# Kernel optimization log

Measured on AMD Instinct MI355X. Metric: run time of the kernel, lower is better.

The kernel has to match this reference:

```python
import jax, jax.numpy as jnp
import numpy as np

# dims: layers, batch, seq_len, num_nodes, n_experts, top_k, expert hidden, pred_len
LAYERS, B, L, N, E, K, DFF, P = 3, 32, 336, 321, 4, 2, 512, 96
LOSS_COEF = 0.01
INV_SQRT2 = 0.7071067811865476


def setup_inputs() -> dict:
    key = jax.random.key(0)
    ks = jax.random.split(key, 10)
    w = lambda k, shape: (jax.random.normal(k, shape, jnp.float32) * 0.02)
    return {
        "x": jax.random.normal(ks[0], (B, L, N, 1), jnp.float32),
        "noise": jax.random.normal(ks[1], (LAYERS, B, E), jnp.float32),
        "w_gate": w(ks[2], (LAYERS, L, E)),
        "w_noise": w(ks[3], (LAYERS, L, E)),
        "W1": w(ks[4], (LAYERS, E, L, DFF)),
        "b1": jnp.zeros((LAYERS, E, DFF), jnp.float32),
        "W2": w(ks[5], (LAYERS, E, DFF, L)),
        "b2": jnp.zeros((LAYERS, E, L), jnp.float32),
        "p1w": w(ks[6], (P, L)),
        "p1b": jnp.zeros((P,), jnp.float32),
        "p2w": w(ks[7], (2 * P, P)),
        "p2b": jnp.zeros((2 * P,), jnp.float32),
    }


def _cv_sq(v):
    # squared coefficient of variation (unbiased var, matches torch .var())
    return jnp.var(v, ddof=1) / (jnp.mean(v) ** 2 + 1e-10)


def _norm_cdf(z):
    return 0.5 * (1.0 + jax.lax.erf(z * jnp.asarray(INV_SQRT2, z.dtype)))


def _ams_layer(x, noise, wg, wn, W1, b1, W2, b2):
    # x: [B, L, N] -> [B, L, N]; noisy top-k gated MoE over the time axis
    g = x.mean(axis=2)                                   # [B, L] gate features
    clean = g @ wg                                       # [B, E]
    nstd = jax.nn.softplus(g @ wn) + 1e-2                # [B, E]
    noisy = clean + noise * nstd                         # [B, E]

    top_logits, top_idx = jax.lax.top_k(noisy, K + 1)    # [B, K+1]
    gates_k = jax.nn.softmax(top_logits[:, :K], axis=-1)
    gates = jnp.zeros_like(noisy).at[
        jnp.arange(noisy.shape[0])[:, None], top_idx[:, :K]
    ].set(gates_k)                                       # dense [B, E], zeros off top-k

    importance = gates.sum(axis=0)
    thr_in = top_logits[:, K][:, None]                   # (k+1)-th value
    thr_out = top_logits[:, K - 1][:, None]              # k-th value
    is_in = noisy > thr_in
    load = jnp.where(
        is_in,
        _norm_cdf((clean - thr_in) / nstd),
        _norm_cdf((clean - thr_out) / nstd),
    ).sum(axis=0)
    aux = LOSS_COEF * (_cv_sq(importance) + _cv_sq(load))

    # experts: per-node MLP along time dim, evaluated densely and combined by gates
    xT = x.transpose(0, 2, 1)                            # [B, N, L]
    h = jax.nn.gelu(jnp.einsum('bnl,eld->ebnd', xT, W1) + b1[:, None, None, :])
    y = jnp.einsum('ebnd,edl->ebnl', h, W2) + b2[:, None, None, :]
    out = jnp.einsum('be,ebnl->bln', gates, y) + x       # residual connection
    return out, aux


def reference(x, noise, w_gate, w_noise, W1, b1, W2, b2, p1w, p1b, p2w, p2b):
    x0 = x[..., 0]                                       # [B, L, N]
    # RevIN norm (affine=False): per-sample, per-node stats over time
    mu = x0.mean(axis=1, keepdims=True)
    sd = jnp.sqrt(x0.var(axis=1, keepdims=True) + 1e-5)
    out = (x0 - mu) / sd

    balance_loss = jnp.asarray(0.0, jnp.float32)
    for l in range(LAYERS):
        out, aux = _ams_layer(out, noise[l], w_gate[l], w_noise[l],
                              W1[l], b1[l], W2[l], b2[l])
        balance_loss = balance_loss + aux

    # projection head: [B, N, L] -> [B, N, 2P] -> [B, P, N, 2]
    h = jnp.tanh(out.transpose(0, 2, 1) @ p1w.T + p1b)
    proj = (h @ p2w.T + p2b).reshape(out.shape[0], N, P, 2).transpose(0, 2, 1, 3)
    mean_out = proj[..., 0]
    std_out = jax.nn.softplus(proj[..., 1]) + 1e-6
    return mean_out, balance_loss, std_out
```

## Files before the change

kernel.cpp:

```cpp
#include <hip/hip_runtime.h>
#include <hip/hip_bf16.h>

#define NLAYERS 3
#define BB 32
#define LL 336
#define LP 352
#define NN 321
#define EE 4
#define DHID 512
#define PP 96
#define STOT (BB*NN*LL)
#define MROWS (BB*NN)
#define BPN ((size_t)BB*PP*NN)

#define F1S 5632
#define E1S 180224
#define F2S 8192
#define E2S 172032

typedef __attribute__((ext_vector_type(8))) short short8;
typedef __attribute__((ext_vector_type(4))) float float4v;

union BF { __hip_bfloat16 h; short s; };

__device__ __forceinline__ short f2b(float f) { BF u; u.h = __float2bfloat16(f); return u.s; }

__device__ __forceinline__ float fast_tanh(float y) {
    float e = __expf(2.0f * y);
    return 1.0f - 2.0f / (e + 1.0f);
}
__device__ __forceinline__ float gelu_f(float x) {
    return 0.5f * x * (1.0f + fast_tanh(0.7978845608028654f * (x + 0.044715f * x * x * x)));
}
__device__ __forceinline__ float softplus_f(float x) {
    return fmaxf(x, 0.0f) + log1pf(expf(-fabsf(x)));
}

__global__ __launch_bounds__(256) void prep_kernel(
    const float* __restrict__ x, const float* __restrict__ W1, const float* __restrict__ W2,
    const float* __restrict__ p1w, const float* __restrict__ p2w,
    float* __restrict__ MU, float* __restrict__ IV, float* __restrict__ LOSS,
    float* __restrict__ G0, short* __restrict__ W1f, short* __restrict__ W2f,
    short* __restrict__ p1wb, short* __restrict__ p2wb)
{
    __shared__ short Ws[64][72];
    __shared__ float Ss[4][64], Sq[4][64];
    int idx = blockIdx.x, tid = threadIdx.x;
    if (idx < 1152) {
        const float* src; int K, D, KS, bx, by, le;
        if (idx < 576) {
            le = idx / 48; int r = idx % 48;
            src = W1 + (size_t)le * LL * DHID;
            K = LL; D = DHID; KS = LP; bx = r % 8; by = r / 8;
        } else {
            int s2 = idx - 576; le = s2 / 48; int r = s2 % 48;
            src = W2 + (size_t)le * DHID * LL;
            K = DHID; D = LL; KS = DHID; bx = r % 6; by = r / 6;
        }
        int d0 = bx * 64, k0 = by * 64;
        #pragma unroll
        for (int i = 0; i < 16; ++i) {
            int lin = tid + i * 256;
            int ki = lin >> 6, dj = lin & 63;
            int k = k0 + ki, d = d0 + dj;
            Ws[ki][dj] = (k < K && d < D) ? f2b(src[(size_t)k * D + d]) : (short)0;
        }
        __syncthreads();
        int di = tid >> 2, d = d0 + di;
        if (d >= D) return;
        #pragma unroll
        for (int kp = 0; kp < 2; ++kp) {
            int kj = ((tid & 3) + 4 * kp) * 8;
            int k = k0 + kj;
            if (k >= KS) continue;
            union { short s[8]; uint4 u; } pk;
            #pragma unroll
            for (int j = 0; j < 8; ++j) pk.s[j] = Ws[kj + j][di];
            int nf = d >> 4;
            int ks = k >> 5;
            int l  = (((k >> 3) & 3) << 4) | (d & 15);
            if (idx < 576) {
                size_t o = (size_t)le * E1S + ((size_t)(nf * 11 + ks) * 64 + l) * 8;
                *(uint4*)&W1f[o] = pk.u;
            } else {
                size_t o = (size_t)le * E2S + ((size_t)(nf * 16 + ks) * 64 + l) * 8;
                *(uint4*)&W2f[o] = pk.u;
            }
        }
    } else if (idx < 1344) {
        int q = idx - 1152;
        int b = q / 6, nt = q % 6;
        if (tid < 56) G0[q * 56 + tid] = 0.0f;
        if (q == 0 && tid < 8) LOSS[tid] = 0.0f;
        int ni = tid & 63, lc = tid >> 6;
        int n = nt * 64 + ni;
        float s = 0.f, ss = 0.f;
        if (n < NN) {
            const float* xp = x + ((size_t)b * LL + lc * 84) * NN + n;
            for (int l = 0; l < 84; ++l, xp += NN) {
                float v = *xp; s += v; ss = fmaf(v, v, ss);
            }
        }
        Ss[lc][ni] = s; Sq[lc][ni] = ss;
        __syncthreads();
        if (lc == 0 && n < NN) {
            float st = ((Ss[0][ni] + Ss[1][ni]) + Ss[2][ni]) + Ss[3][ni];
            float sq = ((Sq[0][ni] + Sq[1][ni]) + Sq[2][ni]) + Sq[3][ni];
            float mu  = st * (1.0f / LL);
            float var = sq * (1.0f / LL) - mu * mu;
            MU[b * NN + n] = mu;
            IV[b * NN + n] = 1.0f / sqrtf(var + 1e-5f);
        }
    } else {
        int i = (idx - 1344) * 256 + tid;
        if (i < PP * LP) {
            int n = i / LP, k = i - n * LP;
            p1wb[i] = (k < LL) ? f2b(p1w[n * LL + k]) : (short)0;
        } else if (i < PP * LP + 2 * PP * PP) {
            int j = i - PP * LP;
            p2wb[j] = f2b(p2w[j]);
        }
    }
}

__global__ __launch_bounds__(256) void revin_tn(
    const float* __restrict__ x, const float* __restrict__ MU, const float* __restrict__ IV,
    float* __restrict__ T, short* __restrict__ Tb16, float* __restrict__ G0)
{
    int b = blockIdx.x, nt = blockIdx.y, lt = blockIdx.z;
    int n0 = nt * 64, l0 = lt * 48;
    __shared__ float Ls[48][65];
    __shared__ float Vs[48][65];
    int tid = threadIdx.x;
    #pragma unroll
    for (int i = 0; i < 12; ++i) {
        int lin = tid + i * 256;
        int li = lin >> 6, ni = lin & 63;
        int n = n0 + ni;
        Ls[li][ni] = (n < NN) ? x[((size_t)b * LL + l0 + li) * NN + n] : 0.f;
    }
    __syncthreads();
    int r = tid >> 2, q = tid & 3;
    int n = n0 + r;
    bool valid = (n < NN);
    float mu = 0.f, iv = 0.f;
    if (valid) { mu = MU[b * NN + n]; iv = IV[b * NN + n]; }
    size_t rowf = (size_t)(b * NN + (valid ? n : 0)) * LL + l0;
    size_t rowb = (size_t)(b * NN + (valid ? n : 0)) * LP + l0;
    #pragma unroll
    for (int k = 0; k < 3; ++k) {
        int c = (q + 4 * k) * 4;
        float4 v;
        v.x = (Ls[c    ][r] - mu) * iv;
        v.y = (Ls[c + 1][r] - mu) * iv;
        v.z = (Ls[c + 2][r] - mu) * iv;
        v.w = (Ls[c + 3][r] - mu) * iv;
        Vs[c][r] = v.x; Vs[c + 1][r] = v.y; Vs[c + 2][r] = v.z; Vs[c + 3][r] = v.w;
        if (valid) {
            *(float4*)&T[rowf + c] = v;
            union { short s[4]; uint2 u; } pk;
            pk.s[0] = f2b(v.x); pk.s[1] = f2b(v.y); pk.s[2] = f2b(v.z); pk.s[3] = f2b(v.w);
            *(uint2*)&Tb16[rowb + c] = pk.u;
        }
    }
    if (valid && lt == 6 && q == 3) {
        size_t base = (size_t)(b * NN + n) * LP;
        *(uint4*)&Tb16[base + 336] = make_uint4(0, 0, 0, 0);
        *(uint4*)&Tb16[base + 344] = make_uint4(0, 0, 0, 0);
    }
    __syncthreads();
    if (tid < 48) {
        float s = 0.f;
        #pragma unroll 8
        for (int rr = 0; rr < 64; ++rr) s += Vs[tid][rr];
        unsafeAtomicAdd(&G0[b * LL + l0 + tid], s);
    }
}

struct LossSM {
    float pc2[BB][EE][2], pn2[BB][EE][2];
    float sc[BB][EE], sn[BB][EE], sy[BB][EE], sg[BB][EE];
    float sti[BB], sto[BB];
    float simp[EE], sload[EE];
};

__device__ void loss_tail(LossSM* S, const float* __restrict__ Gcur, float* __restrict__ Gnext,
                          const float* __restrict__ wgL, const float* __restrict__ wnL,
                          const float* __restrict__ noiseL, float* __restrict__ LOSS, int tid)
{
    __syncthreads();
    for (int t = tid; t < BB * LL; t += 256) Gnext[t] = 0.0f;
    {
        int bb = tid >> 3, ee = (tid >> 1) & 3, sub = tid & 1;
        float c = 0.f, nr = 0.f;
        const float* gp = Gcur + bb * LL;
        for (int l = sub * 168; l < sub * 168 + 168; ++l) {
            float gv = gp[l] * (1.0f / NN);
            c  = fmaf(gv, wgL[l * EE + ee], c);
            nr = fmaf(gv, wnL[l * EE + ee], nr);
        }
        S->pc2[bb][ee][sub] = c; S->pn2[bb][ee][sub] = nr;
    }
    __syncthreads();
    if (tid < 128) {
        int bb = tid >> 2, ee = tid & 3;
        float c  = S->pc2[bb][ee][0] + S->pc2[bb][ee][1];
        float nr = S->pn2[bb][ee][0] + S->pn2[bb][ee][1];
        float ns = softplus_f(nr) + 1e-2f;
        S->sc[bb][ee] = c; S->sn[bb][ee] = ns;
        S->sy[bb][ee] = fmaf(noiseL[bb * EE + ee], ns, c);
    }
    __syncthreads();
    if (tid < 128 && (tid & 3) == 0) {
        int bb = tid >> 2;
        float v[4];
        #pragma unroll
        for (int i = 0; i < 4; ++i) v[i] = S->sy[bb][i];
        int i0 = 0;
        for (int i = 1; i < 4; ++i) if (v[i] > v[i0]) i0 = i;
        int i1 = -1;
        for (int i = 0; i < 4; ++i) { if (i == i0) continue; if (i1 < 0 || v[i] > v[i1]) i1 = i; }
        float m3 = -1e30f;
        for (int i = 0; i < 4; ++i) { if (i == i0 || i == i1) continue; if (v[i] > m3) m3 = v[i]; }
        float e1 = expf(v[i1] - v[i0]);
        float invd = 1.0f / (1.0f + e1);
        #pragma unroll
        for (int i = 0; i < 4; ++i) S->sg[bb][i] = 0.f;
        S->sg[bb][i0] = invd;
        S->sg[bb][i1] = e1 * invd;
        S->sti[bb] = m3;
        S->sto[bb] = v[i1];
    }
    __syncthreads();
    if (tid < EE) {
        int ee = tid;
        float imp = 0.f, ld = 0.f;
        for (int bb2 = 0; bb2 < BB; ++bb2) {
            imp += S->sg[bb2][ee];
            float thr = (S->sy[bb2][ee] > S->sti[bb2]) ? S->sti[bb2] : S->sto[bb2];
            float z = (S->sc[bb2][ee] - thr) / S->sn[bb2][ee];
            ld += 0.5f * (1.0f + erff(z * 0.7071067811865476f));
        }
        S->simp[ee] = imp; S->sload[ee] = ld;
    }
    __syncthreads();
    if (tid == 0) {
        float aux = 0.f;
        {
            float m = (S->simp[0] + S->simp[1] + S->simp[2] + S->simp[3]) * 0.25f;
            float var = 0.f;
            for (int i = 0; i < 4; ++i) { float d = S->simp[i] - m; var += d * d; }
            var *= (1.0f / 3.0f);
            aux += var / (m * m + 1e-10f);
        }
        {
            float m = (S->sload[0] + S->sload[1] + S->sload[2] + S->sload[3]) * 0.25f;
            float var = 0.f;
            for (int i = 0; i < 4; ++i) { float d = S->sload[i] - m; var += d * d; }
            var *= (1.0f / 3.0f);
            aux += var / (m * m + 1e-10f);
        }
        LOSS[0] += 0.01f * aux;
    }
}

__global__ __launch_bounds__(256, 3) void fc1_mfma(
    const short* __restrict__ Tb16, const short* __restrict__ W1f_l,
    const float* __restrict__ b1_l,
    const float* __restrict__ Gcur, float* __restrict__ Gnext,
    const float* __restrict__ wgL, const float* __restrict__ wnL,
    const float* __restrict__ noiseL,
    int* __restrict__ IDX, float* __restrict__ GV,
    short* __restrict__ Hs, float* __restrict__ LOSS)
{
    int i = blockIdx.x;
    int low = i & 7, rest = i >> 3;
    int v = rest & 3, ghi = rest >> 2;
    int g = ghi * 8 + low;
    int y = g % 6, b = g / 6;
    int xt = v & 1, slot = v >> 1;
    int m0 = y * 64, n0 = xt * 256;
    int tid = threadIdx.x;
    int wave = tid >> 6, lane = tid & 63, quad = lane >> 4, l16 = lane & 15;
    __shared__ __align__(16) short Al[64][360];
    __shared__ int sE[2];
    __shared__ float sGt[2];
    {
        int r = tid >> 2, c0 = (tid & 3) * 8;
        const short* src = Tb16 + ((size_t)b * NN + m0 + r) * LP + c0;
        #pragma unroll
        for (int ks = 0; ks < 11; ++ks)
            *(uint4*)&Al[r][c0 + ks * 32] = *(const uint4*)(src + ks * 32);
    }
    if (tid < 64) {
        float pc[4] = {0.f,0.f,0.f,0.f}, pn[4] = {0.f,0.f,0.f,0.f};
        const float* gp = Gcur + b * LL;
        for (int l = tid; l < LL; l += 64) {
            float gv = gp[l] * (1.0f / NN);
            #pragma unroll
            for (int e2 = 0; e2 < 4; ++e2) {
                pc[e2] = fmaf(gv, wgL[l * EE + e2], pc[e2]);
                pn[e2] = fmaf(gv, wnL[l * EE + e2], pn[e2]);
            }
        }
        #pragma unroll
        for (int off = 32; off >= 1; off >>= 1) {
            #pragma unroll
            for (int e2 = 0; e2 < 4; ++e2) {
                pc[e2] += __shfl_xor(pc[e2], off);
                pn[e2] += __shfl_xor(pn[e2], off);
            }
        }
        if (tid == 0) {
            float vv[4];
            #pragma unroll
            for (int e2 = 0; e2 < 4; ++e2) {
                float ns = softplus_f(pn[e2]) + 1e-2f;
                vv[e2] = fmaf(noiseL[b * EE + e2], ns, pc[e2]);
            }
            int i0 = 0;
            for (int e2 = 1; e2 < 4; ++e2) if (vv[e2] > vv[i0]) i0 = e2;
            int i1 = -1;
            for (int e2 = 0; e2 < 4; ++e2) { if (e2 == i0) continue; if (i1 < 0 || vv[e2] > vv[i1]) i1 = e2; }
            float e1v = expf(vv[i1] - vv[i0]);
            float invd = 1.0f / (1.0f + e1v);
            sE[0] = i0; sE[1] = i1; sGt[0] = invd; sGt[1] = e1v * invd;
        }
    }
    __syncthreads();
    int e = sE[slot];
    float gt = sGt[slot];
    if (y == 0 && v == 0 && tid < 2) {
        IDX[2 * b + tid] = sE[tid];
        GV[2 * b + tid] = sGt[tid];
    }

    const short* Bf = W1f_l + (size_t)(e * 32 + xt * 16 + wave * 4) * F1S + lane * 8;
    float4v zero4 = {0.f, 0.f, 0.f, 0.f};
    float4v acc[4][4];
    #pragma unroll
    for (int a = 0; a < 4; ++a)
        #pragma unroll
        for (int j = 0; j < 4; ++j) acc[a][j] = zero4;

    short8 bc0 = *(const short8*)(Bf);
    short8 bc1 = *(const short8*)(Bf + F1S);
    short8 bc2 = *(const short8*)(Bf + 2 * F1S);
    short8 bc3 = *(const short8*)(Bf + 3 * F1S);
    #pragma unroll
    for (int ks = 0; ks < 11; ++ks) {
        short8 bn0, bn1, bn2, bn3;
        if (ks < 10) {
            int o = (ks + 1) * 512;
            bn0 = *(const short8*)(Bf + o);
            bn1 = *(const short8*)(Bf + F1S + o);
            bn2 = *(const short8*)(Bf + 2 * F1S + o);
            bn3 = *(const short8*)(Bf + 3 * F1S + o);
        }
        int off = ks * 32;
        short8 af[4];
        #pragma unroll
        for (int mi = 0; mi < 4; ++mi) af[mi] = *(const short8*)&Al[mi * 16 + l16][off + quad * 8];
        #pragma unroll
        for (int mi = 0; mi < 4; ++mi) {
            acc[mi][0] = __builtin_amdgcn_mfma_f32_16x16x32_bf16(af[mi], bc0, acc[mi][0], 0, 0, 0);
            acc[mi][1] = __builtin_amdgcn_mfma_f32_16x16x32_bf16(af[mi], bc1, acc[mi][1], 0, 0, 0);
            acc[mi][2] = __builtin_amdgcn_mfma_f32_16x16x32_bf16(af[mi], bc2, acc[mi][2], 0, 0, 0);
            acc[mi][3] = __builtin_amdgcn_mfma_f32_16x16x32_bf16(af[mi], bc3, acc[mi][3], 0, 0, 0);
        }
        if (ks < 10) { bc0 = bn0; bc1 = bn1; bc2 = bn2; bc3 = bn3; }
    }
    const float* bb = b1_l + (size_t)e * DHID;
    int wn4 = wave * 64;
    float bias[4];
    #pragma unroll
    for (int ni = 0; ni < 4; ++ni) bias[ni] = bb[n0 + wn4 + ni * 16 + l16];
    short* Ho = Hs + (size_t)(b * 2 + slot) * NN * DHID;
    #pragma unroll
    for (int mi = 0; mi < 4; ++mi) {
        #pragma unroll
        for (int r = 0; r < 4; ++r) {
            int gm = m0 + mi * 16 + quad * 4 + r;
            if (gm >= NN) continue;
            #pragma unroll
            for (int ni = 0; ni < 4; ++ni) {
                int gd = n0 + wn4 + ni * 16 + l16;
                float vv = acc[mi][ni][r] + bias[ni];
                Ho[(size_t)gm * DHID + gd] = f2b(gt * gelu_f(vv));
            }
        }
    }
    if (i == 0) loss_tail((LossSM*)&Al[0][0], Gcur, Gnext, wgL, wnL, noiseL, LOSS, tid);
}

__global__ __launch_bounds__(256, 4) void fc2_fused(
    const short* __restrict__ Hs, const short* __restrict__ W2f_l,
    const float* __restrict__ b2_l, float* __restrict__ T,
    short* __restrict__ Tb16, float* __restrict__ Gnext,
    const int* __restrict__ IDX, const float* __restrict__ GV, int lastL)
{
    int i = blockIdx.x;
    int low = i & 7, rest = i >> 3;
    int v = rest % 3, ghi = rest / 3;
    int g = ghi * 8 + low;
    int y = g % 6, b = g / 6;
    int m0 = y * 64, n0 = v * 128;
    int tid = threadIdx.x;
    int wave = tid >> 6, lane = tid & 63, quad = lane >> 4, l16 = lane & 15;
    int wn = wave * 32;
    __shared__ short Al[64][264];
    int e0 = IDX[2 * b], e1 = IDX[2 * b + 1];
    float gt0 = GV[2 * b], gt1 = GV[2 * b + 1];
    float4v zero4 = {0.f, 0.f, 0.f, 0.f};
    float4v acc[4][2];
    #pragma unroll
    for (int a = 0; a < 4; ++a)
        #pragma unroll
        for (int j = 0; j < 2; ++j) acc[a][j] = zero4;

    int nfr = v * 8 + wave * 2;
    int nf0 = (nfr > 20) ? 20 : nfr;
    int nf1 = (nfr + 1 > 20) ? 20 : nfr + 1;

    int r8 = tid >> 5, c0s = (tid & 31) * 8;
    #pragma unroll
    for (int sc2 = 0; sc2 < 4; ++sc2) {
        int slot = sc2 >> 1, chunk = sc2 & 1;
        int koff = chunk * 256;
        int ez = slot ? e1 : e0;
        const short* As = Hs + ((size_t)(b * 2 + slot) * NN + m0) * DHID + koff;
        #pragma unroll
        for (int a = 0; a < 8; ++a)
            *(uint4*)&Al[a * 8 + r8][c0s] = *(const uint4*)(As + (size_t)(a * 8 + r8) * DHID + c0s);
        __syncthreads();
        const short* B0 = W2f_l + (size_t)ez * E2S + (size_t)nf0 * F2S + (size_t)chunk * 8 * 512 + lane * 8;
        const short* B1 = W2f_l + (size_t)ez * E2S + (size_t)nf1 * F2S + (size_t)chunk * 8 * 512 + lane * 8;
        short8 c0 = *(const short8*)(B0);
        short8 c1 = *(const short8*)(B1);
        #pragma unroll
        for (int ks = 0; ks < 8; ++ks) {
            short8 n0v, n1v;
            if (ks < 7) {
                n0v = *(const short8*)(B0 + (ks + 1) * 512);
                n1v = *(const short8*)(B1 + (ks + 1) * 512);
            }
            int off = ks * 32;
            short8 af[4];
            #pragma unroll
            for (int mi = 0; mi < 4; ++mi) af[mi] = *(const short8*)&Al[mi * 16 + l16][off + quad * 8];
            #pragma unroll
            for (int mi = 0; mi < 4; ++mi) {
                acc[mi][0] = __builtin_amdgcn_mfma_f32_16x16x32_bf16(af[mi], c0, acc[mi][0], 0, 0, 0);
                acc[mi][1] = __builtin_amdgcn_mfma_f32_16x16x32_bf16(af[mi], c1, acc[mi][1], 0, 0, 0);
            }
            if (ks < 7) { c0 = n0v; c1 = n1v; }
        }
        __syncthreads();
    }
    const float* b2e0 = b2_l + (size_t)e0 * LL;
    const float* b2e1 = b2_l + (size_t)e1 * LL;
    float* Tb = T + (size_t)b * NN * LL;
    short* Bt = Tb16 + (size_t)b * NN * LP;
    #pragma unroll
    for (int ni = 0; ni < 2; ++ni) {
        int gl = n0 + wn + ni * 16 + l16;
        float s = 0.f;
        if (gl < LL) {
            float bias = gt0 * b2e0[gl] + gt1 * b2e1[gl];
            #pragma unroll
            for (int mi = 0; mi < 4; ++mi) {
                #pragma unroll
                for (int r = 0; r < 4; ++r) {
                    int gm = m0 + mi * 16 + quad * 4 + r;
                    if (gm < NN) {
                        float vv = acc[mi][ni][r] + bias + Tb[(size_t)gm * LL + gl];
                        if (!lastL) Tb[(size_t)gm * LL + gl] = vv;
                        Bt[(size_t)gm * LP + gl] = f2b(vv);
                        s += vv;
                    }
                }
            }
        }
        s += __shfl_xor(s, 16);
        s += __shfl_xor(s, 32);
        if (!lastL && quad == 0 && gl < LL)
            unsafeAtomicAdd(&Gnext[b * LL + gl], s);
    }
}

__global__ __launch_bounds__(256) void proj_fused(
    const short* __restrict__ Tb16,
    const short* __restrict__ p1wb, const float* __restrict__ p1b,
    const short* __restrict__ p2wb, const float* __restrict__ p2b,
    float* __restrict__ out, const float* __restrict__ LOSS)
{
    __shared__ short Al[32][360];
    __shared__ short Hp[32][104];
    int m0 = blockIdx.x * 32;
    int tid = threadIdx.x;
    if (blockIdx.x == 0 && tid == 0) out[BPN] = LOSS[0];
    int wave = tid >> 6, lane = tid & 63, quad = lane >> 4, l16 = lane & 15;
    float4v zero4 = {0.f, 0.f, 0.f, 0.f};

    #pragma unroll
    for (int i = 0; i < 6; ++i) {
        int idx = tid + i * 256;
        if (idx < 1408) {
            int r = idx / 44, c = (idx - r * 44) * 8;
            *(uint4*)&Al[r][c] = *(const uint4*)(Tb16 + (size_t)(m0 + r) * LP + c);
        }
    }
    __syncthreads();

    {
        int rf = wave & 1, cfb = wave >> 1;
        float4v acc1[3];
        #pragma unroll
        for (int j = 0; j < 3; ++j) acc1[j] = zero4;
        const short* B1p0 = p1wb + (size_t)(cfb * 16 + l16) * LP + quad * 8;
        #pragma unroll
        for (int ks = 0; ks < 11; ++ks) {
            int off = ks * 32;
            short8 af = *(const short8*)&Al[rf * 16 + l16][off + quad * 8];
            #pragma unroll
            for (int j = 0; j < 3; ++j) {
                short8 bf = *(const short8*)(B1p0 + (size_t)j * 32 * LP + off);
                acc1[j] = __builtin_amdgcn_mfma_f32_16x16x32_bf16(af, bf, acc1[j], 0, 0, 0);
            }
        }
        #pragma unroll
        for (int j = 0; j < 3; ++j) {
            int p = (cfb + 2 * j) * 16 + l16;
            float pb = p1b[p];
            #pragma unroll
            for (int r = 0; r < 4; ++r)
                Hp[rf * 16 + quad * 4 + r][p] = f2b(fast_tanh(acc1[j][r] + pb));
        }
    }
    __syncthreads();

    float4v acc2[3][2];
    #pragma unroll
    for (int a = 0; a < 3; ++a)
        #pragma unroll
        for (int j = 0; j < 2; ++j) acc2[a][j] = zero4;
    #pragma unroll
    for (int kc = 0; kc < 3; ++kc) {
        int off = kc * 32 + quad * 8;
        short8 bfv0 = *(const short8*)&Hp[l16][off];
        short8 bfv1 = *(const short8*)&Hp[16 + l16][off];
        #pragma unroll
        for (int mi = 0; mi < 3; ++mi) {
            int cf = wave * 3 + mi;
            short8 af = *(const short8*)(p2wb + (size_t)(cf * 16 + l16) * PP + off);
            acc2[mi][0] = __builtin_amdgcn_mfma_f32_16x16x32_bf16(af, bfv0, acc2[mi][0], 0, 0, 0);
            acc2[mi][1] = __builtin_amdgcn_mfma_f32_16x16x32_bf16(af, bfv1, acc2[mi][1], 0, 0, 0);
        }
    }
    int bqv[2], ndv[2];
    #pragma unroll
    for (int ni = 0; ni < 2; ++ni) {
        int gm = m0 + ni * 16 + l16;
        int bq = gm / NN;
        bqv[ni] = bq; ndv[ni] = gm - bq * NN;
    }
    #pragma unroll
    for (int mi = 0; mi < 3; ++mi) {
        #pragma unroll
        for (int r = 0; r < 4; ++r) {
            int c = (wave * 3 + mi) * 16 + quad * 4 + r;
            float pb = p2b[c];
            int p = c >> 1;
            if ((r & 1) == 0) {
                #pragma unroll
                for (int ni = 0; ni < 2; ++ni) {
                    float v = acc2[mi][ni][r] + pb;
                    out[((size_t)bqv[ni] * PP + p) * NN + ndv[ni]] = v;
                }
            } else {
                #pragma unroll
                for (int ni = 0; ni < 2; ++ni) {
                    float v = acc2[mi][ni][r] + pb;
                    out[BPN + 1 + ((size_t)bqv[ni] * PP + p) * NN + ndv[ni]] = softplus_f(v) + 1e-6f;
                }
            }
        }
    }
}

extern "C" void kernel_launch(void* const* d_in, const int* in_sizes, int n_in,
                              void* d_out, int out_size, void* d_ws, size_t ws_size,
                              hipStream_t stream)
{
    const float* x     = (const float*)d_in[0];
    const float* noise = (const float*)d_in[1];
    const float* wg    = (const float*)d_in[2];
    const float* wn    = (const float*)d_in[3];
    const float* W1    = (const float*)d_in[4];
    const float* b1    = (const float*)d_in[5];
    const float* W2    = (const float*)d_in[6];
    const float* b2    = (const float*)d_in[7];
    const float* p1w   = (const float*)d_in[8];
    const float* p1b   = (const float*)d_in[9];
    const float* p2w   = (const float*)d_in[10];
    const float* p2b   = (const float*)d_in[11];
    float* out = (float*)d_out;

    float* ws   = (float*)d_ws;
    float* T    = ws;
    float* G0   = T + STOT;
    float* G1   = G0 + BB * LL;
    float* LOSS = G1 + BB * LL;
    float* GV   = LOSS + 8;
    int*   IDX  = (int*)(GV + 64);
    float* MU   = (float*)(IDX + 64);
    float* IV   = MU + MROWS;
    short* W1f  = (short*)(IV + MROWS);
    short* W2f  = W1f + (size_t)NLAYERS * EE * DHID * LP;
    short* p1wb = W2f + (size_t)NLAYERS * EE * LL * DHID;
    short* p2wb = p1wb + PP * LP;
    short* Tb16 = p2wb + 2 * PP * PP;
    short* Hs   = Tb16 + (size_t)(MROWS + 64) * LP;

    prep_kernel<<<1549, 256, 0, stream>>>(x, W1, W2, p1w, p2w, MU, IV, LOSS, G0,
                                          W1f, W2f, p1wb, p2wb);
    revin_tn<<<dim3(BB, 6, 7), 256, 0, stream>>>(x, MU, IV, T, Tb16, G0);

    for (int l = 0; l < NLAYERS; ++l) {
        const float* Gcur = (l == 1) ? G1 : G0;
        float* Gnext      = (l == 1) ? G0 : G1;
        fc1_mfma<<<768, 256, 0, stream>>>(
            Tb16, W1f + (size_t)l * EE * E1S, b1 + (size_t)l * EE * DHID,
            Gcur, Gnext, wg + (size_t)l * LL * EE, wn + (size_t)l * LL * EE,
            noise + (size_t)l * BB * EE, IDX, GV, Hs, LOSS);
        fc2_fused<<<576, 256, 0, stream>>>(
            Hs, W2f + (size_t)l * EE * E2S, b2 + (size_t)l * EE * LL,
            T, Tb16, Gnext, IDX, GV, (l == NLAYERS - 1) ? 1 : 0);
    }
    proj_fused<<<321, 256, 0, stream>>>(Tb16, p1wb, p1b, p2wb, p2b, out, LOSS);
}
```

Measured before the change: 347.1 us.

## Parallelize gate reduction and deepen prefetch pipelines in both MoE GEMM kernels

The gate-logit reduction in the first expert GEMM now uses all four waves with a shared-memory cross-wave sum instead of a single wave, and every thread computes top-k redundantly rather than waiting on one thread. The W1 and W2 B-fragment loads are prefetched two k-steps ahead instead of one. In the second GEMM the next A-tile chunk is loaded into registers while the current chunk's MFMAs run, then written to LDS. This is meant to hide global-load latency and shorten the serial gate prologue, at the cost of more registers, which may reduce occupancy.

```diff
diff --git a/kernel.cpp b/kernel.cpp
--- a/kernel.cpp
+++ b/kernel.cpp
@@ -283,8 +283,7 @@
     int tid = threadIdx.x;
     int wave = tid >> 6, lane = tid & 63, quad = lane >> 4, l16 = lane & 15;
     __shared__ __align__(16) short Al[64][360];
-    __shared__ int sE[2];
-    __shared__ float sGt[2];
+    __shared__ float redc[4][4], redn[4][4];
     {
         int r = tid >> 2, c0 = (tid & 3) * 8;
         const short* src = Tb16 + ((size_t)b * NN + m0 + r) * LP + c0;
@@ -292,47 +291,59 @@
         for (int ks = 0; ks < 11; ++ks)
             *(uint4*)&Al[r][c0 + ks * 32] = *(const uint4*)(src + ks * 32);
     }
-    if (tid < 64) {
-        float pc[4] = {0.f,0.f,0.f,0.f}, pn[4] = {0.f,0.f,0.f,0.f};
+    {
+        float pce[4] = {0.f,0.f,0.f,0.f}, pne[4] = {0.f,0.f,0.f,0.f};
         const float* gp = Gcur + b * LL;
-        for (int l = tid; l < LL; l += 64) {
-            float gv = gp[l] * (1.0f / NN);
+        #pragma unroll
+        for (int pass = 0; pass < 2; ++pass) {
+            int l = tid + pass * 256;
+            if (l < LL) {
+                float gv = gp[l] * (1.0f / NN);
+                #pragma unroll
+                for (int e2 = 0; e2 < 4; ++e2) {
+                    pce[e2] = fmaf(gv, wgL[l * EE + e2], pce[e2]);
+                    pne[e2] = fmaf(gv, wnL[l * EE + e2], pne[e2]);
+                }
+            }
+        }
+        #pragma unroll
+        for (int off = 32; off >= 1; off >>= 1) {
             #pragma unroll
             for (int e2 = 0; e2 < 4; ++e2) {
-                pc[e2] = fmaf(gv, wgL[l * EE + e2], pc[e2]);
-                pn[e2] = fmaf(gv, wnL[l * EE + e2], pn[e2]);
-            }
-        }
-        #pragma unroll
-        for (int off = 32; off >= 1; off >>= 1) {
-            #pragma unroll
-            for (int e2 = 0; e2 < 4; ++e2) {
-                pc[e2] += __shfl_xor(pc[e2], off);
-                pn[e2] += __shfl_xor(pn[e2], off);
-            }
-        }
-        if (tid == 0) {
-            float vv[4];
-            #pragma unroll
-            for (int e2 = 0; e2 < 4; ++e2) {
-                float ns = softplus_f(pn[e2]) + 1e-2f;
-                vv[e2] = fmaf(noiseL[b * EE + e2], ns, pc[e2]);
-            }
-            int i0 = 0;
-            for (int e2 = 1; e2 < 4; ++e2) if (vv[e2] > vv[i0]) i0 = e2;
-            int i1 = -1;
-            for (int e2 = 0; e2 < 4; ++e2) { if (e2 == i0) continue; if (i1 < 0 || vv[e2] > vv[i1]) i1 = e2; }
-            float e1v = expf(vv[i1] - vv[i0]);
-            float invd = 1.0f / (1.0f + e1v);
-            sE[0] = i0; sE[1] = i1; sGt[0] = invd; sGt[1] = e1v * invd;
-        }
-    }
-    __syncthreads();
-    int e = sE[slot];
-    float gt = sGt[slot];
-    if (y == 0 && v == 0 && tid < 2) {
-        IDX[2 * b + tid] = sE[tid];
-        GV[2 * b + tid] = sGt[tid];
+                pce[e2] += __shfl_xor(pce[e2], off);
+                pne[e2] += __shfl_xor(pne[e2], off);
+            }
+        }
+        if (lane == 0) {
+            #pragma unroll
+            for (int e2 = 0; e2 < 4; ++e2) { redc[wave][e2] = pce[e2]; redn[wave][e2] = pne[e2]; }
+        }
+    }
+    __syncthreads();
+    int e; float gt;
+    {
+        float vv[4];
+        #pragma unroll
+        for (int e2 = 0; e2 < 4; ++e2) {
+            float c  = ((redc[0][e2] + redc[1][e2]) + redc[2][e2]) + redc[3][e2];
+            float nr = ((redn[0][e2] + redn[1][e2]) + redn[2][e2]) + redn[3][e2];
+            float ns = softplus_f(nr) + 1e-2f;
+            vv[e2] = fmaf(noiseL[b * EE + e2], ns, c);
+        }
+        int i0 = 0;
+        #pragma unroll
+        for (int e2 = 1; e2 < 4; ++e2) if (vv[e2] > vv[i0]) i0 = e2;
+        int i1 = -1;
+        #pragma unroll
+        for (int e2 = 0; e2 < 4; ++e2) { if (e2 == i0) continue; if (i1 < 0 || vv[e2] > vv[i1]) i1 = e2; }
+        float e1v = expf(vv[i1] - vv[i0]);
+        float invd = 1.0f / (1.0f + e1v);
+        e  = slot ? i1 : i0;
+        gt = slot ? (e1v * invd) : invd;
+        if (y == 0 && v == 0 && tid == 0) {
+            IDX[2 * b] = i0; IDX[2 * b + 1] = i1;
+            GV[2 * b] = invd; GV[2 * b + 1] = e1v * invd;
+        }
     }
 
     const short* Bf = W1f_l + (size_t)(e * 32 + xt * 16 + wave * 4) * F1S + lane * 8;
@@ -343,19 +354,18 @@
         #pragma unroll
         for (int j = 0; j < 4; ++j) acc[a][j] = zero4;
 
-    short8 bc0 = *(const short8*)(Bf);
-    short8 bc1 = *(const short8*)(Bf + F1S);
-    short8 bc2 = *(const short8*)(Bf + 2 * F1S);
-    short8 bc3 = *(const short8*)(Bf + 3 * F1S);
+    short8 bc[4], bd[4];
+    #pragma unroll
+    for (int j = 0; j < 4; ++j) bc[j] = *(const short8*)(Bf + j * F1S);
+    #pragma unroll
+    for (int j = 0; j < 4; ++j) bd[j] = *(const short8*)(Bf + j * F1S + 512);
     #pragma unroll
     for (int ks = 0; ks < 11; ++ks) {
-        short8 bn0, bn1, bn2, bn3;
-        if (ks < 10) {
-            int o = (ks + 1) * 512;
-            bn0 = *(const short8*)(Bf + o);
-            bn1 = *(const short8*)(Bf + F1S + o);
-            bn2 = *(const short8*)(Bf + 2 * F1S + o);
-            bn3 = *(const short8*)(Bf + 3 * F1S + o);
+        short8 bn[4];
+        if (ks < 9) {
+            int o = (ks + 2) * 512;
+            #pragma unroll
+            for (int j = 0; j < 4; ++j) bn[j] = *(const short8*)(Bf + j * F1S + o);
         }
         int off = ks * 32;
         short8 af[4];
@@ -363,12 +373,13 @@
         for (int mi = 0; mi < 4; ++mi) af[mi] = *(const short8*)&Al[mi * 16 + l16][off + quad * 8];
         #pragma unroll
         for (int mi = 0; mi < 4; ++mi) {
-            acc[mi][0] = __builtin_amdgcn_mfma_f32_16x16x32_bf16(af[mi], bc0, acc[mi][0], 0, 0, 0);
-            acc[mi][1] = __builtin_amdgcn_mfma_f32_16x16x32_bf16(af[mi], bc1, acc[mi][1], 0, 0, 0);
-            acc[mi][2] = __builtin_amdgcn_mfma_f32_16x16x32_bf16(af[mi], bc2, acc[mi][2], 0, 0, 0);
-            acc[mi][3] = __builtin_amdgcn_mfma_f32_16x16x32_bf16(af[mi], bc3, acc[mi][3], 0, 0, 0);
-        }
-        if (ks < 10) { bc0 = bn0; bc1 = bn1; bc2 = bn2; bc3 = bn3; }
+            acc[mi][0] = __builtin_amdgcn_mfma_f32_16x16x32_bf16(af[mi], bc[0], acc[mi][0], 0, 0, 0);
+            acc[mi][1] = __builtin_amdgcn_mfma_f32_16x16x32_bf16(af[mi], bc[1], acc[mi][1], 0, 0, 0);
+            acc[mi][2] = __builtin_amdgcn_mfma_f32_16x16x32_bf16(af[mi], bc[2], acc[mi][2], 0, 0, 0);
+            acc[mi][3] = __builtin_amdgcn_mfma_f32_16x16x32_bf16(af[mi], bc[3], acc[mi][3], 0, 0, 0);
+        }
+        #pragma unroll
+        for (int j = 0; j < 4; ++j) { bc[j] = bd[j]; if (ks < 9) bd[j] = bn[j]; }
     }
     const float* bb = b1_l + (size_t)e * DHID;
     int wn4 = wave * 64;
@@ -423,26 +434,40 @@
     int nf1 = (nfr + 1 > 20) ? 20 : nfr + 1;
 
     int r8 = tid >> 5, c0s = (tid & 31) * 8;
+    uint4 areg[8];
+    {
+        const short* As = Hs + ((size_t)(b * 2 + 0) * NN + m0) * DHID + 0;
+        #pragma unroll
+        for (int a = 0; a < 8; ++a)
+            areg[a] = *(const uint4*)(As + (size_t)(a * 8 + r8) * DHID + c0s);
+        #pragma unroll
+        for (int a = 0; a < 8; ++a)
+            *(uint4*)&Al[a * 8 + r8][c0s] = areg[a];
+    }
+    __syncthreads();
     #pragma unroll
     for (int sc2 = 0; sc2 < 4; ++sc2) {
         int slot = sc2 >> 1, chunk = sc2 & 1;
-        int koff = chunk * 256;
         int ez = slot ? e1 : e0;
-        const short* As = Hs + ((size_t)(b * 2 + slot) * NN + m0) * DHID + koff;
-        #pragma unroll
-        for (int a = 0; a < 8; ++a)
-            *(uint4*)&Al[a * 8 + r8][c0s] = *(const uint4*)(As + (size_t)(a * 8 + r8) * DHID + c0s);
-        __syncthreads();
-        const short* B0 = W2f_l + (size_t)ez * E2S + (size_t)nf0 * F2S + (size_t)chunk * 8 * 512 + lane * 8;
-        const short* B1 = W2f_l + (size_t)ez * E2S + (size_t)nf1 * F2S + (size_t)chunk * 8 * 512 + lane * 8;
-        short8 c0 = *(const short8*)(B0);
-        short8 c1 = *(const short8*)(B1);
+        if (sc2 < 3) {
+            int nslot = (sc2 + 1) >> 1, nchunk = (sc2 + 1) & 1;
+            const short* Asn = Hs + ((size_t)(b * 2 + nslot) * NN + m0) * DHID + nchunk * 256;
+            #pragma unroll
+            for (int a = 0; a < 8; ++a)
+                areg[a] = *(const uint4*)(Asn + (size_t)(a * 8 + r8) * DHID + c0s);
+        }
+        const short* B0 = W2f_l + (size_t)ez * E2S + (size_t)nf0 * F2S + (size_t)chunk * 4096 + lane * 8;
+        const short* B1 = W2f_l + (size_t)ez * E2S + (size_t)nf1 * F2S + (size_t)chunk * 4096 + lane * 8;
+        short8 c0v = *(const short8*)(B0);
+        short8 c1v = *(const short8*)(B1);
+        short8 d0v = *(const short8*)(B0 + 512);
+        short8 d1v = *(const short8*)(B1 + 512);
         #pragma unroll
         for (int ks = 0; ks < 8; ++ks) {
             short8 n0v, n1v;
-            if (ks < 7) {
-                n0v = *(const short8*)(B0 + (ks + 1) * 512);
-                n1v = *(const short8*)(B1 + (ks + 1) * 512);
+            if (ks < 6) {
+                n0v = *(const short8*)(B0 + (ks + 2) * 512);
+                n1v = *(const short8*)(B1 + (ks + 2) * 512);
             }
             int off = ks * 32;
             short8 af[4];
@@ -450,12 +475,19 @@
             for (int mi = 0; mi < 4; ++mi) af[mi] = *(const short8*)&Al[mi * 16 + l16][off + quad * 8];
             #pragma unroll
             for (int mi = 0; mi < 4; ++mi) {
-                acc[mi][0] = __builtin_amdgcn_mfma_f32_16x16x32_bf16(af[mi], c0, acc[mi][0], 0, 0, 0);
-                acc[mi][1] = __builtin_amdgcn_mfma_f32_16x16x32_bf16(af[mi], c1, acc[mi][1], 0, 0, 0);
-            }
-            if (ks < 7) { c0 = n0v; c1 = n1v; }
+                acc[mi][0] = __builtin_amdgcn_mfma_f32_16x16x32_bf16(af[mi], c0v, acc[mi][0], 0, 0, 0);
+                acc[mi][1] = __builtin_amdgcn_mfma_f32_16x16x32_bf16(af[mi], c1v, acc[mi][1], 0, 0, 0);
+            }
+            c0v = d0v; c1v = d1v;
+            if (ks < 6) { d0v = n0v; d1v = n1v; }
         }
         __syncthreads();
+        if (sc2 < 3) {
+            #pragma unroll
+            for (int a = 0; a < 8; ++a)
+                *(uint4*)&Al[a * 8 + r8][c0s] = areg[a];
+            __syncthreads();
+        }
     }
     const float* b2e0 = b2_l + (size_t)e0 * LL;
     const float* b2e1 = b2_l + (size_t)e1 * LL;
```

After: 406.7 us. 17.2% more time.
